# Optimization experiments

Hardware: AMD Instinct MI355X
Metric: run time of the kernel (lower is better)

## Reference

```python
import jax, jax.numpy as jnp
import numpy as np
from jax.scipy.special import xlogy

NUM_TTA = 64
FILTER_VIEWS = 0.1
KEPT_VIEWS = int(FILTER_VIEWS * NUM_TTA)  # 6
EPS = 1e-8


def setup_inputs() -> dict:
    key = jax.random.key(0)
    k1, k2 = jax.random.split(key)
    x = jax.random.normal(k1, (16384, 4096), dtype=jnp.float32)
    W = jax.random.normal(k2, (4096, 1000), dtype=jnp.float32) * 0.02
    b = jnp.zeros((1000,), dtype=jnp.float32)
    return {"x": x, "W": W, "b": b}


def reference(x, W, b):
    # inner model: linear + softmax -> per-view class probabilities
    probs = jax.nn.softmax(x @ W + b, axis=-1)            # (B*V, C)
    C = probs.shape[-1]
    B = probs.shape[0] // NUM_TTA
    probs = probs.reshape(B, NUM_TTA, C)                  # (b v c)

    # entr(p).sum(-1) == -sum p*log p (entr(0)=0 handled by xlogy)
    entropies = -xlogy(probs, probs).sum(-1)              # (B, V)
    conf_idx = jnp.argsort(entropies, axis=-1)            # most confident first
    votes = jnp.argmax(probs, axis=-1)                    # (B, V)
    sorted_votes = jnp.take_along_axis(votes, conf_idx, axis=1)  # (B, V)

    # initial majority vote over the KEPT_VIEWS most confident views
    counts = jax.nn.one_hot(sorted_votes[:, :KEPT_VIEWS], C, dtype=jnp.float32).sum(1)  # (B, C)

    rows = jnp.arange(B)

    # sequential tie-breaking: while there is a tie at the max, add the next
    # most confident view's vote; at most NUM_TTA - KEPT_VIEWS extra views.
    def body(i, counts):
        maximum = counts.max(axis=-1, keepdims=True)       # (B, 1)
        tied = (counts == maximum).sum(axis=-1) > 1        # (B,)
        cls = sorted_votes[:, KEPT_VIEWS + i]              # (B,)
        return counts.at[rows, cls].add(tied.astype(counts.dtype))

    counts = jax.lax.fori_loop(0, NUM_TTA - KEPT_VIEWS, body, counts)

    predictions = counts / NUM_TTA
    return jnp.log(predictions + EPS)
```

## Files before the change

### kernel.cpp

```cpp
#include <hip/hip_runtime.h>
#include <cstdint>
#include <cstddef>
#include <math.h>

#define M_ROWS 16384
#define N_COLS 1000
#define N_PAD  1024
#define K_DIM  4096
#define NUM_TTA 64
#define KEPT 6
#define BATCH 256
#define CHUNK_MAX 16384
#define NKT (K_DIM / 32)

typedef __attribute__((ext_vector_type(8))) short short8;
typedef __attribute__((ext_vector_type(4))) float v4f;

#define GL_LDS16(g, l)                                                        \
    __builtin_amdgcn_global_load_lds(                                         \
        (const __attribute__((address_space(1))) unsigned int*)(g),           \
        (__attribute__((address_space(3))) unsigned int*)(l), 16, 0, 0)

__device__ __forceinline__ unsigned short bf_rn(float x) {
    unsigned int u = __float_as_uint(x);
    return (unsigned short)((u + 0x7fffu + ((u >> 16) & 1u)) >> 16);
}
__device__ __forceinline__ void split2(float x, unsigned short& h, unsigned short& l) {
    h = bf_rn(x);
    float hf = __uint_as_float(((unsigned int)h) << 16);
    l = bf_rn(x - hf);
}

__global__ __launch_bounds__(1024)
void split_w(const float* __restrict__ W, unsigned short* __restrict__ Wh,
             unsigned short* __restrict__ Wl)
{
    __shared__ float tile[32][33];
    const int k0 = blockIdx.x * 32, n0 = blockIdx.y * 32;
    const int tx = threadIdx.x, ty = threadIdx.y;
    const int n = n0 + tx, k = k0 + ty;
    tile[ty][tx] = (n < N_COLS) ? W[(size_t)k * N_COLS + n] : 0.f;
    __syncthreads();
    const float w = tile[tx][ty];
    unsigned short h, l;
    split2(w, h, l);
    const size_t o = (size_t)(n0 + ty) * K_DIM + k0 + tx;
    Wh[o] = h; Wl[o] = l;
}

__global__ __launch_bounds__(256)
void split_a(const float* __restrict__ x, unsigned short* __restrict__ Ah,
             unsigned short* __restrict__ Al, long long nelem)
{
    const long long i = ((long long)blockIdx.x * 256 + threadIdx.x) * 4;
    if (i >= nelem) return;
    const float4 v = *(const float4*)(x + i);
    unsigned short h0, h1, h2, h3, l0, l1, l2, l3;
    split2(v.x, h0, l0); split2(v.y, h1, l1);
    split2(v.z, h2, l2); split2(v.w, h3, l3);
    ushort4 hv = {h0, h1, h2, h3}, lv = {l0, l1, l2, l3};
    *(ushort4*)(Ah + i) = hv;
    *(ushort4*)(Al + i) = lv;
}

__global__ __launch_bounds__(512, 2)
void gemm_mfma(const unsigned short* __restrict__ Ah, const unsigned short* __restrict__ Al,
               const unsigned short* __restrict__ Bh, const unsigned short* __restrict__ Bl,
               const float* __restrict__ bias, float* __restrict__ logits,
               int m_tiles)
{
    __shared__ __attribute__((aligned(16))) char smem[2 * 4 * 16384];

    const int t    = threadIdx.x;
    const int lane = t & 63;
    const int wave = t >> 6;
    const int wr   = wave >> 2;
    const int wc   = wave & 3;
    const int ml   = lane & 15;
    const int kh   = lane >> 4;

    const int bid  = blockIdx.x;
    const int xcd  = bid & 7;
    const int slot = bid >> 3;
    const int mt   = xcd * (m_tiles >> 3) + (slot >> 2);
    const int nt   = slot & 3;
    const int m0 = mt * 256, n0 = nt * 256;

    const int    schunk = (t & 3) ^ ((t >> 3) & 3);
    const size_t ro     = (size_t)(t >> 2) * (K_DIM * 2) + (size_t)schunk * 16;
    const char* gAh = (const char*)Ah + (size_t)m0 * (K_DIM * 2) + ro;
    const char* gAl = (const char*)Al + (size_t)m0 * (K_DIM * 2) + ro;
    const char* gBh = (const char*)Bh + (size_t)n0 * (K_DIM * 2) + ro;
    const char* gBl = (const char*)Bl + (size_t)n0 * (K_DIM * 2) + ro;
    char* ldst = smem + t * 16;
    const size_t RSTEP = (size_t)128 * K_DIM * 2;

    const int swz = ((kh ^ (ml >> 1)) & 3) << 4;
    const int lbA = wr * 8192 + ml * 64 + swz;
    const int lbB = wc * 4096 + ml * 64 + swz;

    v4f acc[8][4];
#pragma unroll
    for (int i = 0; i < 8; ++i)
#pragma unroll
        for (int j = 0; j < 4; ++j) acc[i][j] = (v4f){0.f, 0.f, 0.f, 0.f};

#define STAGE(WB, KT) do {                                                    \
    const int kb_ = (KT) * 64;                                                \
    char* d_ = ldst + (WB) * 65536;                                           \
    GL_LDS16(gAh + kb_, d_);                GL_LDS16(gAh + RSTEP + kb_, d_ + 8192);  \
    GL_LDS16(gAl + kb_, d_ + 16384);        GL_LDS16(gAl + RSTEP + kb_, d_ + 24576); \
    GL_LDS16(gBh + kb_, d_ + 32768);        GL_LDS16(gBh + RSTEP + kb_, d_ + 40960); \
    GL_LDS16(gBl + kb_, d_ + 49152);        GL_LDS16(gBl + RSTEP + kb_, d_ + 57344); \
} while (0)

#define FRAG(P) (*(const short8*)(smem + (P)))

    STAGE(0, 0);

    short8 ah[4], al[4], bh0[2], bl0[2], bh1[2], bl1[2];

#define MFMA3(AI, NI, AH, AL, BH, BL)                                          \
    acc[AI][NI] = __builtin_amdgcn_mfma_f32_16x16x32_bf16(AH, BL, acc[AI][NI], 0, 0, 0); \
    acc[AI][NI] = __builtin_amdgcn_mfma_f32_16x16x32_bf16(AL, BH, acc[AI][NI], 0, 0, 0); \
    acc[AI][NI] = __builtin_amdgcn_mfma_f32_16x16x32_bf16(AH, BH, acc[AI][NI], 0, 0, 0)

#define TILE_BODY(KT, RB) do {                                                \
    const int B0 = (RB) * 65536;                                              \
    asm volatile("s_waitcnt vmcnt(0)" ::: "memory");                          \
    __builtin_amdgcn_s_barrier();                                             \
    __builtin_amdgcn_sched_barrier(0);                                        \
    if ((KT) + 1 < NKT) STAGE((RB) ^ 1, (KT) + 1);                            \
    _Pragma("unroll")                                                         \
    for (int mf = 0; mf < 4; ++mf) {                                          \
        ah[mf] = FRAG(B0 +         mf * 1024 + lbA);                          \
        al[mf] = FRAG(B0 + 16384 + mf * 1024 + lbA);                          \
    }                                                                         \
    _Pragma("unroll")                                                         \
    for (int nf = 0; nf < 2; ++nf) {                                          \
        bh0[nf] = FRAG(B0 + 32768 + nf * 1024 + lbB);                         \
        bl0[nf] = FRAG(B0 + 49152 + nf * 1024 + lbB);                         \
        bh1[nf] = FRAG(B0 + 32768 + (2 + nf) * 1024 + lbB);                   \
        bl1[nf] = FRAG(B0 + 49152 + (2 + nf) * 1024 + lbB);                   \
    }                                                                         \
    __builtin_amdgcn_s_setprio(1);                                            \
    _Pragma("unroll")                                                         \
    for (int mf = 0; mf < 4; ++mf) {                                          \
        MFMA3(mf, 0, ah[mf], al[mf], bh0[0], bl0[0]);                         \
        MFMA3(mf, 1, ah[mf], al[mf], bh0[1], bl0[1]);                         \
    }                                                                         \
    _Pragma("unroll")                                                         \
    for (int mf = 0; mf < 4; ++mf) {                                          \
        MFMA3(mf, 2, ah[mf], al[mf], bh1[0], bl1[0]);                         \
        MFMA3(mf, 3, ah[mf], al[mf], bh1[1], bl1[1]);                         \
    }                                                                         \
    _Pragma("unroll")                                                         \
    for (int mf = 0; mf < 4; ++mf) {                                          \
        ah[mf] = FRAG(B0 + 4096 +         mf * 1024 + lbA);                   \
        al[mf] = FRAG(B0 + 16384 + 4096 + mf * 1024 + lbA);                   \
    }                                                                         \
    _Pragma("unroll")                                                         \
    for (int mf = 0; mf < 4; ++mf) {                                          \
        MFMA3(4 + mf, 2, ah[mf], al[mf], bh1[0], bl1[0]);                     \
        MFMA3(4 + mf, 3, ah[mf], al[mf], bh1[1], bl1[1]);                     \
    }                                                                         \
    _Pragma("unroll")                                                         \
    for (int mf = 0; mf < 4; ++mf) {                                          \
        MFMA3(4 + mf, 0, ah[mf], al[mf], bh0[0], bl0[0]);                     \
        MFMA3(4 + mf, 1, ah[mf], al[mf], bh0[1], bl0[1]);                     \
    }                                                                         \
    __builtin_amdgcn_s_setprio(0);                                            \
} while (0)

#pragma unroll 1
    for (int kt = 0; kt < NKT; kt += 2) {
        TILE_BODY(kt, 0);
        TILE_BODY(kt + 1, 1);
    }

#pragma unroll
    for (int mi = 0; mi < 8; ++mi) {
        const int rbase = m0 + wr * 128 + (mi >> 2) * 64 + (mi & 3) * 16 + kh * 4;
#pragma unroll
        for (int ni = 0; ni < 4; ++ni) {
            const int col = n0 + wc * 64 + ni * 16 + ml;
            if (col < N_COLS) {
                const float bv = bias[col];
#pragma unroll
                for (int r = 0; r < 4; ++r)
                    logits[(size_t)(rbase + r) * N_COLS + col] = acc[mi][ni][r] + bv;
            }
        }
    }
#undef TILE_BODY
#undef MFMA3
#undef FRAG
#undef STAGE
}

__device__ __forceinline__ double exp_neg(double d) {
    if (d < -700.0) return 0.0;
    const double kd = rint(d * 1.4426950408889634074);
    double r = fma(-kd, 6.93147180369123816490e-01, d);
    r = fma(-kd, 1.90821492927058770002e-10, r);
    double p = 2.08767569878680989792e-09;
    p = fma(p, r, 2.50521083854417187751e-08);
    p = fma(p, r, 2.75573192239858906526e-07);
    p = fma(p, r, 2.75573192239858925110e-06);
    p = fma(p, r, 2.48015873015873015873e-05);
    p = fma(p, r, 1.98412698412698412526e-04);
    p = fma(p, r, 1.38888888888888894069e-03);
    p = fma(p, r, 8.33333333333333321769e-03);
    p = fma(p, r, 4.16666666666666643537e-02);
    p = fma(p, r, 1.66666666666666657415e-01);
    p = fma(p, r, 5.0e-01);
    p = fma(p, r, 1.0);
    p = fma(p, r, 1.0);
    const long long k = (long long)kd;
    return p * __longlong_as_double((1023LL + k) << 52);
}

__global__ __launch_bounds__(256)
void row_stats(const float* __restrict__ logits, double* __restrict__ ent,
               int* __restrict__ votes, int v_base)
{
    const int lane = threadIdx.x & 63;
    const int wave = threadIdx.x >> 6;
    const int row  = blockIdx.x * 4 + wave;
    const float* rp = logits + (size_t)row * N_COLS;

    float v[16];
    float bv = -3.0e38f; int bi = 0;
#pragma unroll
    for (int j = 0; j < 16; ++j) {
        const int c = j * 64 + lane;
        const float x = (c < N_COLS) ? rp[c] : -3.0e38f;
        v[j] = x;
        if (x > bv) { bv = x; bi = c; }
    }
#pragma unroll
    for (int s = 32; s > 0; s >>= 1) {
        const float ov = __shfl_xor(bv, s);
        const int   oi = __shfl_xor(bi, s);
        if (ov > bv || (ov == bv && oi < bi)) { bv = ov; bi = oi; }
    }
    const float mx = bv;
    const int amax = bi;

    double S = 0.0, T = 0.0;
#pragma unroll
    for (int j = 0; j < 16; ++j) {
        const int c = j * 64 + lane;
        if (c < N_COLS) {
            const float d = v[j] - mx;
            const double e = exp_neg((double)d);
            S += e; T += e * (double)d;
        }
    }
#pragma unroll
    for (int s = 32; s > 0; s >>= 1) {
        S += __shfl_xor(S, s);
        T += __shfl_xor(T, s);
    }
    if (lane == 0) {
        ent[v_base + row]   = log(S) - T / S;
        votes[v_base + row] = amax;
    }
}

__global__ __launch_bounds__(64)
void vote_kernel(const double* __restrict__ ent, const int* __restrict__ votes,
                 float* __restrict__ out)
{
    __shared__ double e[NUM_TTA];
    __shared__ int    sv[NUM_TTA];
    __shared__ float  counts[N_COLS];

    const int b = blockIdx.x;
    const int t = threadIdx.x;

    e[t] = ent[b * NUM_TTA + t];
    const int myv = votes[b * NUM_TTA + t];
    for (int c = t; c < N_COLS; c += NUM_TTA) counts[c] = 0.f;
    __syncthreads();

    const double et = e[t];
    int rank = 0;
#pragma unroll
    for (int i = 0; i < NUM_TTA; ++i) {
        const double ei = e[i];
        rank += (ei < et) || (ei == et && i < t);
    }
    sv[rank] = myv;
    __syncthreads();

    if (t == 0) {
        for (int j = 0; j < KEPT; ++j) counts[sv[j]] += 1.f;
        float Mv = 0.f; int Tc = 0;
        for (int j = 0; j < KEPT; ++j) {
            const int c = sv[j];
            bool dup = false;
            for (int q = 0; q < j; ++q) dup = dup || (sv[q] == c);
            if (dup) continue;
            const float cv = counts[c];
            if (cv > Mv) { Mv = cv; Tc = 1; }
            else if (cv == Mv) { Tc += 1; }
        }
        for (int i = 0; i < NUM_TTA - KEPT; ++i) {
            if (Tc <= 1) break;
            const int c = sv[KEPT + i];
            const float oldc = counts[c];
            counts[c] = oldc + 1.f;
            if (oldc == Mv)            { Mv += 1.f; Tc = 1; }
            else if (oldc + 1.f == Mv) { Tc += 1; }
        }
    }
    __syncthreads();

    const size_t o0 = (size_t)b * N_COLS;
    for (int c = t; c < N_COLS; c += NUM_TTA)
        out[o0 + c] = logf(counts[c] * (1.f / 64.f) + 1e-8f);
}

extern "C" void kernel_launch(void* const* d_in, const int* in_sizes, int n_in,
                              void* d_out, int out_size, void* d_ws, size_t ws_size,
                              hipStream_t stream) {
    const float* x    = (const float*)d_in[0];
    const float* Wm   = (const float*)d_in[1];
    const float* bias = (const float*)d_in[2];
    float* out = (float*)d_out;

    char* p = (char*)d_ws;
    double* ent  = (double*)p;                     p += (size_t)M_ROWS * 8;
    int*   votes = (int*)p;                        p += (size_t)M_ROWS * 4;
    unsigned short* Wh = (unsigned short*)p;       p += (size_t)N_PAD * K_DIM * 2;
    unsigned short* Wl = (unsigned short*)p;       p += (size_t)N_PAD * K_DIM * 2;
    const size_t base = (size_t)(p - (char*)d_ws);

    long long R = 0;
    if (ws_size > base) R = (long long)((ws_size - base) / (size_t)(8192 + 8192 + 4000));
    R = (R / 2048) * 2048;
    if (R > CHUNK_MAX) R = CHUNK_MAX;
    if (R < 2048) R = 2048;

    unsigned short* Ah = (unsigned short*)p;
    unsigned short* Al = Ah + (size_t)R * K_DIM;
    float* logits = (float*)(Al + (size_t)R * K_DIM);

    split_w<<<dim3(K_DIM / 32, N_PAD / 32), dim3(32, 32), 0, stream>>>(Wm, Wh, Wl);

    for (int m0 = 0; m0 < M_ROWS; m0 += (int)R) {
        const int rows = (int)(((long long)(M_ROWS - m0) < R) ? (M_ROWS - m0) : R);
        const int m_tiles = rows / 256;
        const long long nel = (long long)rows * K_DIM;
        split_a<<<(int)((nel / 4 + 255) / 256), 256, 0, stream>>>(
            x + (size_t)m0 * K_DIM, Ah, Al, nel);
        gemm_mfma<<<4 * m_tiles, 512, 0, stream>>>(
            Ah, Al, Wh, Wl, bias, logits, m_tiles);
        row_stats<<<rows / 4, 256, 0, stream>>>(logits, ent, votes, m0);
    }
    vote_kernel<<<BATCH, NUM_TTA, 0, stream>>>(ent, votes, out);
}
```

Baseline: 723.6 us.

## Fuse fp32-to-bf16 split of activations into GEMM A-tile loading

Removes the separate split_a kernel and its bf16 hi/lo workspace buffers. The GEMM now reads fp32 x directly into registers, splits it into hi/lo bf16 and writes it to LDS, overlapped with the MFMA work. It also interleaves LDS fragment loads with the MFMAs. This saves the extra global round trip for A (a write plus re-read of 2x bf16). The cost is more VALU work and register pressure in the GEMM, with fp32 A being re-read by each of the four N-tile blocks and the A split repeated per block.

```diff
diff --git a/kernel.cpp b/kernel.cpp
--- a/kernel.cpp
+++ b/kernel.cpp
@@ -29,6 +29,19 @@
     h = bf_rn(x);
     float hf = __uint_as_float(((unsigned int)h) << 16);
     l = bf_rn(x - hf);
+}
+
+__device__ __forceinline__ void split8(const float4& a, const float4& b,
+                                       short8& hv, short8& lv) {
+    unsigned short h, l;
+    split2(a.x, h, l); hv[0] = (short)h; lv[0] = (short)l;
+    split2(a.y, h, l); hv[1] = (short)h; lv[1] = (short)l;
+    split2(a.z, h, l); hv[2] = (short)h; lv[2] = (short)l;
+    split2(a.w, h, l); hv[3] = (short)h; lv[3] = (short)l;
+    split2(b.x, h, l); hv[4] = (short)h; lv[4] = (short)l;
+    split2(b.y, h, l); hv[5] = (short)h; lv[5] = (short)l;
+    split2(b.z, h, l); hv[6] = (short)h; lv[6] = (short)l;
+    split2(b.w, h, l); hv[7] = (short)h; lv[7] = (short)l;
 }
 
 __global__ __launch_bounds__(1024)
@@ -48,24 +61,9 @@
     Wh[o] = h; Wl[o] = l;
 }
 
-__global__ __launch_bounds__(256)
-void split_a(const float* __restrict__ x, unsigned short* __restrict__ Ah,
-             unsigned short* __restrict__ Al, long long nelem)
-{
-    const long long i = ((long long)blockIdx.x * 256 + threadIdx.x) * 4;
-    if (i >= nelem) return;
-    const float4 v = *(const float4*)(x + i);
-    unsigned short h0, h1, h2, h3, l0, l1, l2, l3;
-    split2(v.x, h0, l0); split2(v.y, h1, l1);
-    split2(v.z, h2, l2); split2(v.w, h3, l3);
-    ushort4 hv = {h0, h1, h2, h3}, lv = {l0, l1, l2, l3};
-    *(ushort4*)(Ah + i) = hv;
-    *(ushort4*)(Al + i) = lv;
-}
-
 __global__ __launch_bounds__(512, 2)
-void gemm_mfma(const unsigned short* __restrict__ Ah, const unsigned short* __restrict__ Al,
-               const unsigned short* __restrict__ Bh, const unsigned short* __restrict__ Bl,
+void gemm_mfma(const float* __restrict__ X,
+               const unsigned short* __restrict__ Bh_, const unsigned short* __restrict__ Bl_,
                const float* __restrict__ bias, float* __restrict__ logits,
                int m_tiles)
 {
@@ -88,12 +86,19 @@
 
     const int    schunk = (t & 3) ^ ((t >> 3) & 3);
     const size_t ro     = (size_t)(t >> 2) * (K_DIM * 2) + (size_t)schunk * 16;
-    const char* gAh = (const char*)Ah + (size_t)m0 * (K_DIM * 2) + ro;
-    const char* gAl = (const char*)Al + (size_t)m0 * (K_DIM * 2) + ro;
-    const char* gBh = (const char*)Bh + (size_t)n0 * (K_DIM * 2) + ro;
-    const char* gBl = (const char*)Bl + (size_t)n0 * (K_DIM * 2) + ro;
+    const char* gBh = (const char*)Bh_ + (size_t)n0 * (K_DIM * 2) + ro;
+    const char* gBl = (const char*)Bl_ + (size_t)n0 * (K_DIM * 2) + ro;
     char* ldst = smem + t * 16;
     const size_t RSTEP = (size_t)128 * K_DIM * 2;
+
+    const int ar    = t >> 1;
+    const int ahalf = t & 1;
+    const float* gA = X + (size_t)(m0 + ar) * K_DIM + ahalf * 16;
+    const int sig = (ar >> 1) & 3;
+    const int s0  = (ahalf * 2) ^ sig;
+    const int s1  = (ahalf * 2 + 1) ^ sig;
+    const int aw0 = ar * 64 + (s0 << 4);
+    const int aw1 = ar * 64 + (s1 << 4);
 
     const int swz = ((kh ^ (ml >> 1)) & 3) << 4;
     const int lbA = wr * 8192 + ml * 64 + swz;
@@ -105,70 +110,130 @@
 #pragma unroll
         for (int j = 0; j < 4; ++j) acc[i][j] = (v4f){0.f, 0.f, 0.f, 0.f};
 
-#define STAGE(WB, KT) do {                                                    \
-    const int kb_ = (KT) * 64;                                                \
-    char* d_ = ldst + (WB) * 65536;                                           \
-    GL_LDS16(gAh + kb_, d_);                GL_LDS16(gAh + RSTEP + kb_, d_ + 8192);  \
-    GL_LDS16(gAl + kb_, d_ + 16384);        GL_LDS16(gAl + RSTEP + kb_, d_ + 24576); \
-    GL_LDS16(gBh + kb_, d_ + 32768);        GL_LDS16(gBh + RSTEP + kb_, d_ + 40960); \
-    GL_LDS16(gBl + kb_, d_ + 49152);        GL_LDS16(gBl + RSTEP + kb_, d_ + 57344); \
-} while (0)
-
 #define FRAG(P) (*(const short8*)(smem + (P)))
-
-    STAGE(0, 0);
-
-    short8 ah[4], al[4], bh0[2], bl0[2], bh1[2], bl1[2];
 
 #define MFMA3(AI, NI, AH, AL, BH, BL)                                          \
     acc[AI][NI] = __builtin_amdgcn_mfma_f32_16x16x32_bf16(AH, BL, acc[AI][NI], 0, 0, 0); \
     acc[AI][NI] = __builtin_amdgcn_mfma_f32_16x16x32_bf16(AL, BH, acc[AI][NI], 0, 0, 0); \
     acc[AI][NI] = __builtin_amdgcn_mfma_f32_16x16x32_bf16(AH, BH, acc[AI][NI], 0, 0, 0)
 
+    short8 ah[4], al[4], bh0[2], bl0[2], bh1[2], bl1[2];
+
+    {
+        const float4 fa = *(const float4*)(gA);
+        const float4 fb = *(const float4*)(gA + 4);
+        const float4 fc = *(const float4*)(gA + 8);
+        const float4 fd = *(const float4*)(gA + 12);
+        GL_LDS16(gBh,         ldst + 32768);
+        GL_LDS16(gBh + RSTEP, ldst + 40960);
+        GL_LDS16(gBl,         ldst + 49152);
+        GL_LDS16(gBl + RSTEP, ldst + 57344);
+        short8 hv, lv;
+        split8(fa, fb, hv, lv);
+        *(short8*)(smem + aw0) = hv;
+        *(short8*)(smem + 16384 + aw0) = lv;
+        split8(fc, fd, hv, lv);
+        *(short8*)(smem + aw1) = hv;
+        *(short8*)(smem + 16384 + aw1) = lv;
+    }
+    __syncthreads();
+
 #define TILE_BODY(KT, RB) do {                                                \
     const int B0 = (RB) * 65536;                                              \
-    asm volatile("s_waitcnt vmcnt(0)" ::: "memory");                          \
+    const int B1 = ((RB) ^ 1) * 65536;                                        \
+    asm volatile("s_waitcnt vmcnt(0) lgkmcnt(0)" ::: "memory");               \
     __builtin_amdgcn_s_barrier();                                             \
     __builtin_amdgcn_sched_barrier(0);                                        \
-    if ((KT) + 1 < NKT) STAGE((RB) ^ 1, (KT) + 1);                            \
-    _Pragma("unroll")                                                         \
-    for (int mf = 0; mf < 4; ++mf) {                                          \
-        ah[mf] = FRAG(B0 +         mf * 1024 + lbA);                          \
-        al[mf] = FRAG(B0 + 16384 + mf * 1024 + lbA);                          \
+    const bool pf = (KT) + 1 < NKT;                                           \
+    float4 fa, fb;                                                            \
+    if (pf) {       \
+        const float* ga_ = gA + ((KT) + 1) * 32;                              \
+        fa = *(const float4*)(ga_);                                           \
+        fb = *(const float4*)(ga_ + 4);                                       \
+        const int kb_ = ((KT) + 1) * 64;                                      \
+        GL_LDS16(gBh + kb_,         ldst + B1 + 32768);                       \
+        GL_LDS16(gBh + RSTEP + kb_, ldst + B1 + 40960);                       \
+        GL_LDS16(gBl + kb_,         ldst + B1 + 49152);                       \
+        GL_LDS16(gBl + RSTEP + kb_, ldst + B1 + 57344);                       \
     }                                                                         \
-    _Pragma("unroll")                                                         \
-    for (int nf = 0; nf < 2; ++nf) {                                          \
-        bh0[nf] = FRAG(B0 + 32768 + nf * 1024 + lbB);                         \
-        bl0[nf] = FRAG(B0 + 49152 + nf * 1024 + lbB);                         \
-        bh1[nf] = FRAG(B0 + 32768 + (2 + nf) * 1024 + lbB);                   \
-        bl1[nf] = FRAG(B0 + 49152 + (2 + nf) * 1024 + lbB);                   \
+    \
+    bh0[0] = FRAG(B0 + 32768 + 0 * 1024 + lbB);                               \
+    bl0[0] = FRAG(B0 + 49152 + 0 * 1024 + lbB);                               \
+    bh0[1] = FRAG(B0 + 32768 + 1 * 1024 + lbB);                               \
+    bl0[1] = FRAG(B0 + 49152 + 1 * 1024 + lbB);                               \
+    ah[0] = FRAG(B0 +         0 * 1024 + lbA);                                \
+    al[0] = FRAG(B0 + 16384 + 0 * 1024 + lbA);                                \
+    ah[1] = FRAG(B0 +         1 * 1024 + lbA);                                \
+    al[1] = FRAG(B0 + 16384 + 1 * 1024 + lbA);                                \
+    __builtin_amdgcn_s_setprio(1);                                            \
+    MFMA3(0, 0, ah[0], al[0], bh0[0], bl0[0]);                                \
+    MFMA3(0, 1, ah[0], al[0], bh0[1], bl0[1]);                                \
+    ah[2] = FRAG(B0 +         2 * 1024 + lbA);                                \
+    al[2] = FRAG(B0 + 16384 + 2 * 1024 + lbA);                                \
+    MFMA3(1, 0, ah[1], al[1], bh0[0], bl0[0]);                                \
+    MFMA3(1, 1, ah[1], al[1], bh0[1], bl0[1]);                                \
+    ah[3] = FRAG(B0 +         3 * 1024 + lbA);                                \
+    al[3] = FRAG(B0 + 16384 + 3 * 1024 + lbA);                                \
+    MFMA3(2, 0, ah[2], al[2], bh0[0], bl0[0]);                                \
+    MFMA3(2, 1, ah[2], al[2], bh0[1], bl0[1]);                                \
+    bh1[0] = FRAG(B0 + 32768 + 2 * 1024 + lbB);                               \
+    bl1[0] = FRAG(B0 + 49152 + 2 * 1024 + lbB);                               \
+    bh1[1] = FRAG(B0 + 32768 + 3 * 1024 + lbB);                               \
+    bl1[1] = FRAG(B0 + 49152 + 3 * 1024 + lbB);                               \
+    MFMA3(3, 0, ah[3], al[3], bh0[0], bl0[0]);                                \
+    MFMA3(3, 1, ah[3], al[3], bh0[1], bl0[1]);                                \
+    MFMA3(0, 2, ah[0], al[0], bh1[0], bl1[0]);                                \
+    MFMA3(0, 3, ah[0], al[0], bh1[1], bl1[1]);                                \
+    MFMA3(1, 2, ah[1], al[1], bh1[0], bl1[0]);                                \
+    MFMA3(1, 3, ah[1], al[1], bh1[1], bl1[1]);                                \
+    __builtin_amdgcn_s_setprio(0);                                            \
+    if (pf) {           \
+        short8 hv, lv;                                                        \
+        split8(fa, fb, hv, lv);                                               \
+        *(short8*)(smem + B1 + aw0) = hv;                                     \
+        *(short8*)(smem + B1 + 16384 + aw0) = lv;                             \
+        const float* ga_ = gA + ((KT) + 1) * 32 + 8;                          \
+        fa = *(const float4*)(ga_);                                           \
+        fb = *(const float4*)(ga_ + 4);                                       \
     }                                                                         \
     __builtin_amdgcn_s_setprio(1);                                            \
-    _Pragma("unroll")                                                         \
-    for (int mf = 0; mf < 4; ++mf) {                                          \
-        MFMA3(mf, 0, ah[mf], al[mf], bh0[0], bl0[0]);                         \
-        MFMA3(mf, 1, ah[mf], al[mf], bh0[1], bl0[1]);                         \
+    MFMA3(2, 2, ah[2], al[2], bh1[0], bl1[0]);                                \
+    MFMA3(2, 3, ah[2], al[2], bh1[1], bl1[1]);                                \
+    MFMA3(3, 2, ah[3], al[3], bh1[0], bl1[0]);                                \
+    MFMA3(3, 3, ah[3], al[3], bh1[1], bl1[1]);                                \
+      \
+    ah[0] = FRAG(B0 + 4096 +         0 * 1024 + lbA);                         \
+    al[0] = FRAG(B0 + 4096 + 16384 + 0 * 1024 + lbA);                         \
+    ah[1] = FRAG(B0 + 4096 +         1 * 1024 + lbA);                         \
+    al[1] = FRAG(B0 + 4096 + 16384 + 1 * 1024 + lbA);                         \
+    ah[2] = FRAG(B0 + 4096 +         2 * 1024 + lbA);                         \
+    al[2] = FRAG(B0 + 4096 + 16384 + 2 * 1024 + lbA);                         \
+    ah[3] = FRAG(B0 + 4096 +         3 * 1024 + lbA);                         \
+    al[3] = FRAG(B0 + 4096 + 16384 + 3 * 1024 + lbA);                         \
+    MFMA3(4, 2, ah[0], al[0], bh1[0], bl1[0]);                                \
+    MFMA3(4, 3, ah[0], al[0], bh1[1], bl1[1]);                                \
+    MFMA3(5, 2, ah[1], al[1], bh1[0], bl1[0]);                                \
+    MFMA3(5, 3, ah[1], al[1], bh1[1], bl1[1]);                                \
+    MFMA3(6, 2, ah[2], al[2], bh1[0], bl1[0]);                                \
+    MFMA3(6, 3, ah[2], al[2], bh1[1], bl1[1]);                                \
+    MFMA3(7, 2, ah[3], al[3], bh1[0], bl1[0]);                                \
+    MFMA3(7, 3, ah[3], al[3], bh1[1], bl1[1]);                                \
+    __builtin_amdgcn_s_setprio(0);                                            \
+    if (pf) {                                 \
+        short8 hv, lv;                                                        \
+        split8(fa, fb, hv, lv);                                               \
+        *(short8*)(smem + B1 + aw1) = hv;                                     \
+        *(short8*)(smem + B1 + 16384 + aw1) = lv;                             \
     }                                                                         \
-    _Pragma("unroll")                                                         \
-    for (int mf = 0; mf < 4; ++mf) {                                          \
-        MFMA3(mf, 2, ah[mf], al[mf], bh1[0], bl1[0]);                         \
-        MFMA3(mf, 3, ah[mf], al[mf], bh1[1], bl1[1]);                         \
-    }                                                                         \
-    _Pragma("unroll")                                                         \
-    for (int mf = 0; mf < 4; ++mf) {                                          \
-        ah[mf] = FRAG(B0 + 4096 +         mf * 1024 + lbA);                   \
-        al[mf] = FRAG(B0 + 16384 + 4096 + mf * 1024 + lbA);                   \
-    }                                                                         \
-    _Pragma("unroll")                                                         \
-    for (int mf = 0; mf < 4; ++mf) {                                          \
-        MFMA3(4 + mf, 2, ah[mf], al[mf], bh1[0], bl1[0]);                     \
-        MFMA3(4 + mf, 3, ah[mf], al[mf], bh1[1], bl1[1]);                     \
-    }                                                                         \
-    _Pragma("unroll")                                                         \
-    for (int mf = 0; mf < 4; ++mf) {                                          \
-        MFMA3(4 + mf, 0, ah[mf], al[mf], bh0[0], bl0[0]);                     \
-        MFMA3(4 + mf, 1, ah[mf], al[mf], bh0[1], bl0[1]);                     \
-    }                                                                         \
+    __builtin_amdgcn_s_setprio(1);                                            \
+    MFMA3(4, 0, ah[0], al[0], bh0[0], bl0[0]);                                \
+    MFMA3(4, 1, ah[0], al[0], bh0[1], bl0[1]);                                \
+    MFMA3(5, 0, ah[1], al[1], bh0[0], bl0[0]);                                \
+    MFMA3(5, 1, ah[1], al[1], bh0[1], bl0[1]);                                \
+    MFMA3(6, 0, ah[2], al[2], bh0[0], bl0[0]);                                \
+    MFMA3(6, 1, ah[2], al[2], bh0[1], bl0[1]);                                \
+    MFMA3(7, 0, ah[3], al[3], bh0[0], bl0[0]);                                \
+    MFMA3(7, 1, ah[3], al[3], bh0[1], bl0[1]);                                \
     __builtin_amdgcn_s_setprio(0);                                            \
 } while (0)
 
@@ -195,7 +260,6 @@
 #undef TILE_BODY
 #undef MFMA3
 #undef FRAG
-#undef STAGE
 }
 
 __device__ __forceinline__ double exp_neg(double d) {
@@ -338,25 +402,20 @@
     const size_t base = (size_t)(p - (char*)d_ws);
 
     long long R = 0;
-    if (ws_size > base) R = (long long)((ws_size - base) / (size_t)(8192 + 8192 + 4000));
+    if (ws_size > base) R = (long long)((ws_size - base) / (size_t)4000);
     R = (R / 2048) * 2048;
     if (R > CHUNK_MAX) R = CHUNK_MAX;
     if (R < 2048) R = 2048;
 
-    unsigned short* Ah = (unsigned short*)p;
-    unsigned short* Al = Ah + (size_t)R * K_DIM;
-    float* logits = (float*)(Al + (size_t)R * K_DIM);
+    float* logits = (float*)p;
 
     split_w<<<dim3(K_DIM / 32, N_PAD / 32), dim3(32, 32), 0, stream>>>(Wm, Wh, Wl);
 
     for (int m0 = 0; m0 < M_ROWS; m0 += (int)R) {
         const int rows = (int)(((long long)(M_ROWS - m0) < R) ? (M_ROWS - m0) : R);
         const int m_tiles = rows / 256;
-        const long long nel = (long long)rows * K_DIM;
-        split_a<<<(int)((nel / 4 + 255) / 256), 256, 0, stream>>>(
-            x + (size_t)m0 * K_DIM, Ah, Al, nel);
         gemm_mfma<<<4 * m_tiles, 512, 0, stream>>>(
-            Ah, Al, Wh, Wl, bias, logits, m_tiles);
+            x + (size_t)m0 * K_DIM, Wh, Wl, bias, logits, m_tiles);
         row_stats<<<rows / 4, 256, 0, stream>>>(logits, ent, votes, m0);
     }
     vote_kernel<<<BATCH, NUM_TTA, 0, stream>>>(ent, votes, out);
```

Result: faster. 666.9 us (-7.8%).
